# Performance work log

Measured on AMD Instinct MI355X. Metric: run time of the kernel, lower is better.

## Reference

```python
import jax, jax.numpy as jnp
import numpy as np

D_HEAD = 64  # module's self.heads scaling constant


def setup_inputs() -> dict:
    key = jax.random.key(0)
    kq, kk, kv = jax.random.split(key, 3)
    N, HW, C = 4, 4096, 64
    Q = jax.random.normal(kq, (N, HW, C), dtype=jnp.float32)
    K = jax.random.normal(kk, (N, HW, C), dtype=jnp.float32)
    V = jax.random.normal(kv, (N, HW, C), dtype=jnp.float32)
    return {"Q": Q, "K": K, "V": V}


def reference(Q, K, V):
    # logits[n, q, k] = Q[n,q,:] . K[n,k,:] / sqrt(d_head)
    scale = 1.0 / jnp.sqrt(jnp.asarray(D_HEAD, dtype=Q.dtype))
    logits = jnp.einsum("nqc,nkc->nqk", Q, K) * scale  # [N, HW, HW]
    # NOTE: softmax over the QUERY axis (dim=1), non-standard
    attn = jax.nn.softmax(logits, axis=1)
    return jnp.einsum("nqk,nkc->nqc", attn, V)
```

## Files before the change

### kernel.cpp

```cpp
#include <hip/hip_runtime.h>
#include <hip/hip_bf16.h>

#define NB 4
#define HWN 4096
#define CD 64
#define NSTRIDE (HWN * CD)

typedef short short8 __attribute__((ext_vector_type(8), may_alias));
typedef short short4v __attribute__((ext_vector_type(4), may_alias));
typedef float f32x4 __attribute__((ext_vector_type(4), may_alias));

__device__ constexpr float C1 = 0.18033688011112042f;

__device__ __forceinline__ unsigned short f2bf(float f) {
    unsigned u = __builtin_bit_cast(unsigned, f);
    u = (u + 0x7FFFu + ((u >> 16) & 1u)) >> 16;
    return (unsigned short)u;
}

__device__ __forceinline__ float fexp2(float x) {
#if __has_builtin(__builtin_amdgcn_exp2f)
    return __builtin_amdgcn_exp2f(x);
#else
    return exp2f(x);
#endif
}

__device__ __forceinline__ unsigned pk2(float a, float b) {
    __hip_bfloat162 h = __float22bfloat162_rn(float2{a, b});
    unsigned u;
    __builtin_memcpy(&u, &h, 4);
    return u;
}

__device__ __forceinline__ size_t qk_swz(int row, int c) {
    return (size_t)(row >> 4) * 1024 + (c >> 5) * 512 +
           ((((c >> 3) & 3) * 16 + (row & 15)) * 8) + (c & 7);
}

__global__ __launch_bounds__(256) void cvt_qk(const float* __restrict__ Q,
                                              const float* __restrict__ K,
                                              unsigned short* __restrict__ Qs,
                                              unsigned short* __restrict__ Ks) {
    int i = (blockIdx.x * 256 + threadIdx.x) * 4;
    int rg = i >> 6, c = i & 63;
    int n = rg >> 12, r = rg & 4095;
    float4 q = *(const float4*)(Q + i);
    float4 k = *(const float4*)(K + i);
    ushort4 qo, ko;
    qo.x = f2bf(q.x * C1); qo.y = f2bf(q.y * C1);
    qo.z = f2bf(q.z * C1); qo.w = f2bf(q.w * C1);
    ko.x = f2bf(k.x); ko.y = f2bf(k.y); ko.z = f2bf(k.z); ko.w = f2bf(k.w);
    size_t off = (size_t)n * NSTRIDE + qk_swz(r, c);
    *(ushort4*)(Qs + off) = qo;
    *(ushort4*)(Ks + off) = ko;
}

__global__ __attribute__((amdgpu_flat_work_group_size(256, 256), amdgpu_waves_per_eu(2, 4)))
void lsum_kernel(const unsigned short* __restrict__ Qs,
                 const unsigned short* __restrict__ Ks,
                 float* __restrict__ l) {
    int tid = threadIdx.x;
    int w = tid >> 6, lane = tid & 63, quad = lane >> 4, m16 = lane & 15;
    int n = blockIdx.y;
    int kbase = blockIdx.x * 256 + w * 64;

    const unsigned short* Kp = Ks + (size_t)n * NSTRIDE + (kbase >> 4) * 1024 + lane * 8;
    short8 ka0 = *(const short8*)(Kp);
    short8 ka1 = *(const short8*)(Kp + 512);
    short8 kb0 = *(const short8*)(Kp + 1024);
    short8 kb1 = *(const short8*)(Kp + 1536);
    short8 kc0 = *(const short8*)(Kp + 2048);
    short8 kc1 = *(const short8*)(Kp + 2560);
    short8 kd0 = *(const short8*)(Kp + 3072);
    short8 kd1 = *(const short8*)(Kp + 3584);

    const unsigned short* Qp = Qs + (size_t)n * NSTRIDE + blockIdx.z * 16384 + lane * 8;

    short8 qc0 = *(const short8*)(Qp);
    short8 qc1 = *(const short8*)(Qp + 512);
    Qp += 1024;

    float lA[4] = {0.f, 0.f, 0.f, 0.f};
    float lB[4] = {0.f, 0.f, 0.f, 0.f};
    float lC[4] = {0.f, 0.f, 0.f, 0.f};
    float lD[4] = {0.f, 0.f, 0.f, 0.f};
#pragma unroll 2
    for (int qc = 0; qc < 16; ++qc) {
        short8 qn0 = *(const short8*)(Qp);
        short8 qn1 = *(const short8*)(Qp + 512);
        f32x4 a = {0.f, 0.f, 0.f, 0.f}, b = a, c = a, d = a;
        a = __builtin_amdgcn_mfma_f32_16x16x32_bf16(ka0, qc0, a, 0, 0, 0);
        a = __builtin_amdgcn_mfma_f32_16x16x32_bf16(ka1, qc1, a, 0, 0, 0);
        b = __builtin_amdgcn_mfma_f32_16x16x32_bf16(kb0, qc0, b, 0, 0, 0);
        b = __builtin_amdgcn_mfma_f32_16x16x32_bf16(kb1, qc1, b, 0, 0, 0);
        c = __builtin_amdgcn_mfma_f32_16x16x32_bf16(kc0, qc0, c, 0, 0, 0);
        c = __builtin_amdgcn_mfma_f32_16x16x32_bf16(kc1, qc1, c, 0, 0, 0);
        d = __builtin_amdgcn_mfma_f32_16x16x32_bf16(kd0, qc0, d, 0, 0, 0);
        d = __builtin_amdgcn_mfma_f32_16x16x32_bf16(kd1, qc1, d, 0, 0, 0);
#pragma unroll
        for (int r = 0; r < 4; ++r) {
            lA[r] += fexp2(a[r]);
            lB[r] += fexp2(b[r]);
            lC[r] += fexp2(c[r]);
            lD[r] += fexp2(d[r]);
        }
        qc0 = qn0; qc1 = qn1;
        Qp += 1024;
    }
#pragma unroll
    for (int r = 0; r < 4; ++r)
        for (int d1 = 1; d1 < 16; d1 <<= 1) {
            lA[r] += __shfl_xor(lA[r], d1);
            lB[r] += __shfl_xor(lB[r], d1);
            lC[r] += __shfl_xor(lC[r], d1);
            lD[r] += __shfl_xor(lD[r], d1);
        }
    if (m16 == 0) {
        float* lp = l + n * HWN + kbase + quad * 4;
#pragma unroll
        for (int r = 0; r < 4; ++r) {
            atomicAdd(lp + r, lA[r]);
            atomicAdd(lp + 16 + r, lB[r]);
            atomicAdd(lp + 32 + r, lC[r]);
            atomicAdd(lp + 48 + r, lD[r]);
        }
    }
}

__global__ __launch_bounds__(256) void prep_v(const float* __restrict__ V,
                                              const float* __restrict__ l,
                                              unsigned short* __restrict__ Vts) {
    __shared__ float rl[64];
    __shared__ float tile[64][65];
    int tid = threadIdx.x, n = blockIdx.y, kbase = blockIdx.x * 64;
    if (tid < 64) rl[tid] = 1.0f / l[n * HWN + kbase + tid];
    __syncthreads();
#pragma unroll
    for (int i = 0; i < 16; ++i) {
        int e = i * 256 + tid;
        int k = e >> 6, c = e & 63;
        tile[c][k] = V[((size_t)(n * HWN + kbase + k)) * CD + c] * rl[k];
    }
    __syncthreads();
#pragma unroll
    for (int i = 0; i < 2; ++i) {
        int s = i * 256 + tid;
        int kb32 = s >> 8;
        int ct = (s >> 6) & 3;
        int ll = s & 63;
        int cc = ct * 16 + (ll & 15);
        int kq = ((ll >> 4) & 3) * 4;
        int k0 = kb32 * 32 + kq;
        short8 v;
#pragma unroll
        for (int j = 0; j < 4; ++j) {
            v[j]     = (short)f2bf(tile[cc][k0 + j]);
            v[4 + j] = (short)f2bf(tile[cc][k0 + 16 + j]);
        }
        size_t off = (size_t)n * NSTRIDE + (size_t)((kbase >> 5) + kb32) * 2048 +
                     ct * 512 + ll * 8;
        *(short8*)(Vts + off) = v;
    }
}

__global__ __attribute__((amdgpu_flat_work_group_size(256, 256), amdgpu_waves_per_eu(2, 4)))
void attn_kernel(const unsigned short* __restrict__ Qs,
                 const unsigned short* __restrict__ Ks,
                 const unsigned short* __restrict__ Vts,
                 float* __restrict__ partial,
                 int nit) {
    int tid = threadIdx.x;
    int w = tid >> 6, lane = tid & 63, quad = lane >> 4, m16 = lane & 15;
    int n = blockIdx.y;
    int qbase = blockIdx.x * 128 + w * 16;

    const unsigned short* Qp = Qs + (size_t)n * NSTRIDE + (qbase >> 4) * 1024 + lane * 8;
    short8 qa0 = *(const short8*)(Qp);
    short8 qa1 = *(const short8*)(Qp + 512);
    short8 qb0 = *(const short8*)(Qp + 4096);
    short8 qb1 = *(const short8*)(Qp + 4096 + 512);

    size_t kofs = (size_t)blockIdx.z * (size_t)nit * 2048;
    const unsigned short* Kp = Ks + (size_t)n * NSTRIDE + kofs + lane * 8;
    const unsigned short* Vp = Vts + (size_t)n * NSTRIDE + kofs + lane * 8;

    f32x4 oA[4], oB[4];
#pragma unroll
    for (int ct = 0; ct < 4; ++ct) { oA[ct] = f32x4{0.f, 0.f, 0.f, 0.f}; oB[ct] = oA[ct]; }

#pragma unroll 2
    for (int it = 0; it < nit; ++it) {
        short8 kf00 = *(const short8*)(Kp);
        short8 kf01 = *(const short8*)(Kp + 512);
        short8 kf10 = *(const short8*)(Kp + 1024);
        short8 kf11 = *(const short8*)(Kp + 1536);
        f32x4 s00 = {0.f, 0.f, 0.f, 0.f}, s01 = s00, s10 = s00, s11 = s00;
        s00 = __builtin_amdgcn_mfma_f32_16x16x32_bf16(kf00, qa0, s00, 0, 0, 0);
        s00 = __builtin_amdgcn_mfma_f32_16x16x32_bf16(kf01, qa1, s00, 0, 0, 0);
        s01 = __builtin_amdgcn_mfma_f32_16x16x32_bf16(kf10, qa0, s01, 0, 0, 0);
        s01 = __builtin_amdgcn_mfma_f32_16x16x32_bf16(kf11, qa1, s01, 0, 0, 0);
        s10 = __builtin_amdgcn_mfma_f32_16x16x32_bf16(kf00, qb0, s10, 0, 0, 0);
        s10 = __builtin_amdgcn_mfma_f32_16x16x32_bf16(kf01, qb1, s10, 0, 0, 0);
        s11 = __builtin_amdgcn_mfma_f32_16x16x32_bf16(kf10, qb0, s11, 0, 0, 0);
        s11 = __builtin_amdgcn_mfma_f32_16x16x32_bf16(kf11, qb1, s11, 0, 0, 0);

        uint2 w00, w01, w10, w11;
        w00.x = pk2(fexp2(s00[0]), fexp2(s00[1])); w00.y = pk2(fexp2(s00[2]), fexp2(s00[3]));
        w01.x = pk2(fexp2(s01[0]), fexp2(s01[1])); w01.y = pk2(fexp2(s01[2]), fexp2(s01[3]));
        w10.x = pk2(fexp2(s10[0]), fexp2(s10[1])); w10.y = pk2(fexp2(s10[2]), fexp2(s10[3]));
        w11.x = pk2(fexp2(s11[0]), fexp2(s11[1])); w11.y = pk2(fexp2(s11[2]), fexp2(s11[3]));
        short4v pA0 = __builtin_bit_cast(short4v, w00);
        short4v pA1 = __builtin_bit_cast(short4v, w01);
        short4v pB0 = __builtin_bit_cast(short4v, w10);
        short4v pB1 = __builtin_bit_cast(short4v, w11);

#pragma unroll
        for (int ct = 0; ct < 4; ++ct) {
            short8 vf = *(const short8*)(Vp + ct * 512);
            short4v vlo = __builtin_shufflevector(vf, vf, 0, 1, 2, 3);
            short4v vhi = __builtin_shufflevector(vf, vf, 4, 5, 6, 7);
            oA[ct] = __builtin_amdgcn_mfma_f32_16x16x16bf16_1k(vlo, pA0, oA[ct], 0, 0, 0);
            oA[ct] = __builtin_amdgcn_mfma_f32_16x16x16bf16_1k(vhi, pA1, oA[ct], 0, 0, 0);
            oB[ct] = __builtin_amdgcn_mfma_f32_16x16x16bf16_1k(vlo, pB0, oB[ct], 0, 0, 0);
            oB[ct] = __builtin_amdgcn_mfma_f32_16x16x16bf16_1k(vhi, pB1, oB[ct], 0, 0, 0);
        }
        Kp += 2048;
        Vp += 2048;
    }

    float* ppA = partial + (size_t)blockIdx.z * (NB * HWN * CD) +
                 ((size_t)(n * HWN + qbase + m16)) * CD + quad * 4;
    float* ppB = ppA + (size_t)64 * CD;
#pragma unroll
    for (int ct = 0; ct < 4; ++ct) {
        *(f32x4*)(ppA + ct * 16) = oA[ct];
        *(f32x4*)(ppB + ct * 16) = oB[ct];
    }
}

__global__ __launch_bounds__(256) void reduce_out(const float* __restrict__ p,
                                                  float* __restrict__ out, int ns) {
    int i = (blockIdx.x * 256 + threadIdx.x) * 4;
    f32x4 a = *(const f32x4*)(p + i);
    for (int s = 1; s < ns; ++s)
        a = a + *(const f32x4*)(p + (size_t)s * (NB * HWN * CD) + i);
    *(f32x4*)(out + i) = a;
}

extern "C" void kernel_launch(void* const* d_in, const int* in_sizes, int n_in,
                              void* d_out, int out_size, void* d_ws, size_t ws_size,
                              hipStream_t stream) {
    const float* Q = (const float*)d_in[0];
    const float* K = (const float*)d_in[1];
    const float* V = (const float*)d_in[2];
    float* out = (float*)d_out;

    char* ws = (char*)d_ws;
    unsigned short* Qs  = (unsigned short*)(ws);
    unsigned short* Ks  = (unsigned short*)(ws + (1u << 21));
    unsigned short* Vts = (unsigned short*)(ws + (2u << 21));
    float* l       = (float*)(ws + (3u << 21));
    float* partial = (float*)(ws + (4u << 21));

    size_t base = (size_t)(4u << 21);
    size_t slice = (size_t)NB * HWN * CD * sizeof(float);
    int ns = (ws_size >= base + 8 * slice) ? 8
           : (ws_size >= base + 4 * slice) ? 4 : 2;
    int nit = HWN / ns / 32;

    (void)hipMemsetAsync(l, 0, (size_t)NB * HWN * sizeof(float), stream);

    cvt_qk<<<1024, 256, 0, stream>>>(Q, K, Qs, Ks);
    lsum_kernel<<<dim3(16, NB, 16), 256, 0, stream>>>(Qs, Ks, l);
    prep_v<<<dim3(64, NB), 256, 0, stream>>>(V, l, Vts);
    attn_kernel<<<dim3(32, NB, ns), 256, 0, stream>>>(Qs, Ks, Vts, partial, nit);
    reduce_out<<<1024, 256, 0, stream>>>(partial, out, ns);
}
```

Before: 113.7 us.

## Prefetch K/V fragments, add MFMA priority hints, fold l-zeroing into conversion kernel

```diff
diff --git a/kernel.cpp b/kernel.cpp
--- a/kernel.cpp
+++ b/kernel.cpp
@@ -41,7 +41,12 @@
 __global__ __launch_bounds__(256) void cvt_qk(const float* __restrict__ Q,
                                               const float* __restrict__ K,
                                               unsigned short* __restrict__ Qs,
-                                              unsigned short* __restrict__ Ks) {
+                                              unsigned short* __restrict__ Ks,
+                                              float* __restrict__ l) {
+    if (blockIdx.x < 16) {
+        int zi = blockIdx.x * 256 + threadIdx.x;
+        *(f32x4*)(l + (size_t)zi * 4) = f32x4{0.f, 0.f, 0.f, 0.f};
+    }
     int i = (blockIdx.x * 256 + threadIdx.x) * 4;
     int rg = i >> 6, c = i & 63;
     int n = rg >> 12, r = rg & 4095;
@@ -90,6 +95,7 @@
         short8 qn0 = *(const short8*)(Qp);
         short8 qn1 = *(const short8*)(Qp + 512);
         f32x4 a = {0.f, 0.f, 0.f, 0.f}, b = a, c = a, d = a;
+        __builtin_amdgcn_s_setprio(1);
         a = __builtin_amdgcn_mfma_f32_16x16x32_bf16(ka0, qc0, a, 0, 0, 0);
         a = __builtin_amdgcn_mfma_f32_16x16x32_bf16(ka1, qc1, a, 0, 0, 0);
         b = __builtin_amdgcn_mfma_f32_16x16x32_bf16(kb0, qc0, b, 0, 0, 0);
@@ -98,6 +104,7 @@
         c = __builtin_amdgcn_mfma_f32_16x16x32_bf16(kc1, qc1, c, 0, 0, 0);
         d = __builtin_amdgcn_mfma_f32_16x16x32_bf16(kd0, qc0, d, 0, 0, 0);
         d = __builtin_amdgcn_mfma_f32_16x16x32_bf16(kd1, qc1, d, 0, 0, 0);
+        __builtin_amdgcn_s_setprio(0);
 #pragma unroll
         for (int r = 0; r < 4; ++r) {
             lA[r] += fexp2(a[r]);
@@ -189,13 +196,24 @@
 #pragma unroll
     for (int ct = 0; ct < 4; ++ct) { oA[ct] = f32x4{0.f, 0.f, 0.f, 0.f}; oB[ct] = oA[ct]; }
 
+    short8 kf00 = *(const short8*)(Kp);
+    short8 kf01 = *(const short8*)(Kp + 512);
+    short8 kf10 = *(const short8*)(Kp + 1024);
+    short8 kf11 = *(const short8*)(Kp + 1536);
+
 #pragma unroll 2
     for (int it = 0; it < nit; ++it) {
-        short8 kf00 = *(const short8*)(Kp);
-        short8 kf01 = *(const short8*)(Kp + 512);
-        short8 kf10 = *(const short8*)(Kp + 1024);
-        short8 kf11 = *(const short8*)(Kp + 1536);
+        short8 kn00 = *(const short8*)(Kp + 2048);
+        short8 kn01 = *(const short8*)(Kp + 2560);
+        short8 kn10 = *(const short8*)(Kp + 3072);
+        short8 kn11 = *(const short8*)(Kp + 3584);
+        short8 vf0 = *(const short8*)(Vp);
+        short8 vf1 = *(const short8*)(Vp + 512);
+        short8 vf2 = *(const short8*)(Vp + 1024);
+        short8 vf3 = *(const short8*)(Vp + 1536);
+
         f32x4 s00 = {0.f, 0.f, 0.f, 0.f}, s01 = s00, s10 = s00, s11 = s00;
+        __builtin_amdgcn_s_setprio(1);
         s00 = __builtin_amdgcn_mfma_f32_16x16x32_bf16(kf00, qa0, s00, 0, 0, 0);
         s00 = __builtin_amdgcn_mfma_f32_16x16x32_bf16(kf01, qa1, s00, 0, 0, 0);
         s01 = __builtin_amdgcn_mfma_f32_16x16x32_bf16(kf10, qa0, s01, 0, 0, 0);
@@ -204,6 +222,7 @@
         s10 = __builtin_amdgcn_mfma_f32_16x16x32_bf16(kf01, qb1, s10, 0, 0, 0);
         s11 = __builtin_amdgcn_mfma_f32_16x16x32_bf16(kf10, qb0, s11, 0, 0, 0);
         s11 = __builtin_amdgcn_mfma_f32_16x16x32_bf16(kf11, qb1, s11, 0, 0, 0);
+        __builtin_amdgcn_s_setprio(0);
 
         uint2 w00, w01, w10, w11;
         w00.x = pk2(fexp2(s00[0]), fexp2(s00[1])); w00.y = pk2(fexp2(s00[2]), fexp2(s00[3]));
@@ -215,16 +234,37 @@
         short4v pB0 = __builtin_bit_cast(short4v, w10);
         short4v pB1 = __builtin_bit_cast(short4v, w11);
 
-#pragma unroll
-        for (int ct = 0; ct < 4; ++ct) {
-            short8 vf = *(const short8*)(Vp + ct * 512);
-            short4v vlo = __builtin_shufflevector(vf, vf, 0, 1, 2, 3);
-            short4v vhi = __builtin_shufflevector(vf, vf, 4, 5, 6, 7);
-            oA[ct] = __builtin_amdgcn_mfma_f32_16x16x16bf16_1k(vlo, pA0, oA[ct], 0, 0, 0);
-            oA[ct] = __builtin_amdgcn_mfma_f32_16x16x16bf16_1k(vhi, pA1, oA[ct], 0, 0, 0);
-            oB[ct] = __builtin_amdgcn_mfma_f32_16x16x16bf16_1k(vlo, pB0, oB[ct], 0, 0, 0);
-            oB[ct] = __builtin_amdgcn_mfma_f32_16x16x16bf16_1k(vhi, pB1, oB[ct], 0, 0, 0);
-        }
+        __builtin_amdgcn_s_setprio(1);
+        {
+            short4v vlo, vhi;
+            vlo = __builtin_shufflevector(vf0, vf0, 0, 1, 2, 3);
+            vhi = __builtin_shufflevector(vf0, vf0, 4, 5, 6, 7);
+            oA[0] = __builtin_amdgcn_mfma_f32_16x16x16bf16_1k(vlo, pA0, oA[0], 0, 0, 0);
+            oA[0] = __builtin_amdgcn_mfma_f32_16x16x16bf16_1k(vhi, pA1, oA[0], 0, 0, 0);
+            oB[0] = __builtin_amdgcn_mfma_f32_16x16x16bf16_1k(vlo, pB0, oB[0], 0, 0, 0);
+            oB[0] = __builtin_amdgcn_mfma_f32_16x16x16bf16_1k(vhi, pB1, oB[0], 0, 0, 0);
+            vlo = __builtin_shufflevector(vf1, vf1, 0, 1, 2, 3);
+            vhi = __builtin_shufflevector(vf1, vf1, 4, 5, 6, 7);
+            oA[1] = __builtin_amdgcn_mfma_f32_16x16x16bf16_1k(vlo, pA0, oA[1], 0, 0, 0);
+            oA[1] = __builtin_amdgcn_mfma_f32_16x16x16bf16_1k(vhi, pA1, oA[1], 0, 0, 0);
+            oB[1] = __builtin_amdgcn_mfma_f32_16x16x16bf16_1k(vlo, pB0, oB[1], 0, 0, 0);
+            oB[1] = __builtin_amdgcn_mfma_f32_16x16x16bf16_1k(vhi, pB1, oB[1], 0, 0, 0);
+            vlo = __builtin_shufflevector(vf2, vf2, 0, 1, 2, 3);
+            vhi = __builtin_shufflevector(vf2, vf2, 4, 5, 6, 7);
+            oA[2] = __builtin_amdgcn_mfma_f32_16x16x16bf16_1k(vlo, pA0, oA[2], 0, 0, 0);
+            oA[2] = __builtin_amdgcn_mfma_f32_16x16x16bf16_1k(vhi, pA1, oA[2], 0, 0, 0);
+            oB[2] = __builtin_amdgcn_mfma_f32_16x16x16bf16_1k(vlo, pB0, oB[2], 0, 0, 0);
+            oB[2] = __builtin_amdgcn_mfma_f32_16x16x16bf16_1k(vhi, pB1, oB[2], 0, 0, 0);
+            vlo = __builtin_shufflevector(vf3, vf3, 0, 1, 2, 3);
+            vhi = __builtin_shufflevector(vf3, vf3, 4, 5, 6, 7);
+            oA[3] = __builtin_amdgcn_mfma_f32_16x16x16bf16_1k(vlo, pA0, oA[3], 0, 0, 0);
+            oA[3] = __builtin_amdgcn_mfma_f32_16x16x16bf16_1k(vhi, pA1, oA[3], 0, 0, 0);
+            oB[3] = __builtin_amdgcn_mfma_f32_16x16x16bf16_1k(vlo, pB0, oB[3], 0, 0, 0);
+            oB[3] = __builtin_amdgcn_mfma_f32_16x16x16bf16_1k(vhi, pB1, oB[3], 0, 0, 0);
+        }
+        __builtin_amdgcn_s_setprio(0);
+
+        kf00 = kn00; kf01 = kn01; kf10 = kn10; kf11 = kn11;
         Kp += 2048;
         Vp += 2048;
     }
@@ -269,9 +309,7 @@
            : (ws_size >= base + 4 * slice) ? 4 : 2;
     int nit = HWN / ns / 32;
 
-    (void)hipMemsetAsync(l, 0, (size_t)NB * HWN * sizeof(float), stream);
-
-    cvt_qk<<<1024, 256, 0, stream>>>(Q, K, Qs, Ks);
+    cvt_qk<<<1024, 256, 0, stream>>>(Q, K, Qs, Ks, l);
     lsum_kernel<<<dim3(16, NB, 16), 256, 0, stream>>>(Qs, Ks, l);
     prep_v<<<dim3(64, NB), 256, 0, stream>>>(V, l, Vts);
     attn_kernel<<<dim3(32, NB, ns), 256, 0, stream>>>(Qs, Ks, Vts, partial, nit);
```

New measurement: 110.3 us. 3.0% less time.
